# Performance work log

Hardware: AMD Instinct MI355X
Metric: run time of the kernel (lower is better)

Reference implementation:

```python
import jax, jax.numpy as jnp
import numpy as np

N = 50000
E = 1600000
EPS = 1e-16


def transformer_conv(x, src, dst, ea, Wq, bq, Wk, bk, Wv, bv, We, Ws, bs):
    # PyG TransformerConv, heads=1, concat=True, root_weight=True
    C = Wq.shape[1]
    q = x @ Wq + bq                      # [N, C]
    k = x @ Wk + bk                      # [N, C]
    v = x @ Wv + bv                      # [N, C]
    e = ea @ We                          # [E, C]
    k_e = k[src] + e                     # per-edge key
    v_e = v[src] + e                     # per-edge value
    score = (q[dst] * k_e).sum(-1) / jnp.sqrt(jnp.asarray(C, x.dtype))  # [E]
    # segment softmax over incoming edges of each dst node
    m = jax.ops.segment_max(score, dst, num_segments=N)
    ex = jnp.exp(score - m[dst])
    denom = jax.ops.segment_sum(ex, dst, num_segments=N)
    alpha = ex / (denom[dst] + EPS)
    out = jax.ops.segment_sum(alpha[:, None] * v_e, dst, num_segments=N)
    return out + x @ Ws + bs             # skip connection


def gcn_conv(x, src, dst, W, b):
    # PyG GCNConv: self-loops + symmetric deg^-1/2 normalization
    n_idx = jnp.arange(N)
    src2 = jnp.concatenate([src, n_idx])
    dst2 = jnp.concatenate([dst, n_idx])
    deg = jax.ops.segment_sum(jnp.ones(E + N, x.dtype), dst2, num_segments=N)
    dinv = jnp.where(deg > 0, jax.lax.rsqrt(deg), 0.0)
    norm = dinv[src2] * dinv[dst2]       # [E+N]
    h = x @ W                            # [N, out]
    out = jax.ops.segment_sum(norm[:, None] * h[src2], dst2, num_segments=N)
    return out + b


def setup_inputs() -> dict:
    key = jax.random.key(0)
    ks = jax.random.split(key, 32)
    d = {}
    d['x'] = jax.random.normal(ks[0], (N, 128), jnp.float32)
    d['edge_index'] = jax.random.randint(ks[1], (2, E), 0, N, jnp.int64)
    d['edge_attr'] = jax.random.normal(ks[2], (E, 16), jnp.float32)
    shapes = dict(
        Wq1=(128, 96), bq1=(96,), Wk1=(128, 96), bk1=(96,), Wv1=(128, 96), bv1=(96,),
        We1=(16, 96), Ws1=(128, 96), bs1=(96,),
        Wq2=(96, 64), bq2=(64,), Wk2=(96, 64), bk2=(64,), Wv2=(96, 64), bv2=(64,),
        We2=(16, 64), Ws2=(96, 64), bs2=(64,),
        Wmu=(64, 32), bmu=(32,), Wls=(64, 32), bls=(32,))
    for i, (name, shp) in enumerate(shapes.items()):
        scale = 1.0 / np.sqrt(shp[0]) if len(shp) == 2 else 0.02
        d[name] = jax.random.normal(ks[3 + i], shp, jnp.float32) * scale
    return d


def reference(x, edge_index, edge_attr,
              Wq1, bq1, Wk1, bk1, Wv1, bv1, We1, Ws1, bs1,
              Wq2, bq2, Wk2, bk2, Wv2, bv2, We2, Ws2, bs2,
              Wmu, bmu, Wls, bls):
    src, dst = edge_index[0], edge_index[1]
    h = jax.nn.relu(transformer_conv(x, src, dst, edge_attr,
                                     Wq1, bq1, Wk1, bk1, Wv1, bv1, We1, Ws1, bs1))
    h = jax.nn.relu(transformer_conv(h, src, dst, edge_attr,
                                     Wq2, bq2, Wk2, bk2, Wv2, bv2, We2, Ws2, bs2))
    mu = gcn_conv(h, src, dst, Wmu, bmu)
    logstd = gcn_conv(h, src, dst, Wls, bls)
    return mu, logstd
```

## Files before the change

### kernel.cpp

```cpp
#include <hip/hip_runtime.h>
#include <math.h>


#define TPB 256
#define NGRP 8
typedef unsigned int uint32;
typedef unsigned long long u64;
typedef unsigned short u16;
typedef __attribute__((ext_vector_type(4))) float f32x4;
typedef __attribute__((ext_vector_type(4))) uint32 u32x4;
typedef __attribute__((ext_vector_type(4))) int i32x4;
typedef __attribute__((ext_vector_type(8))) short bf16x8;

__device__ __forceinline__ uint32 f2bf(float f) {
    uint32 u = __float_as_uint(f);
    return (u + 0x7fffu + ((u >> 16) & 1u)) >> 16;
}
__device__ __forceinline__ float bf2f(uint32 b) { return __uint_as_float(b << 16); }

__global__ void hist_kernel(const int* __restrict__ dst, int* __restrict__ deg,
                            int E, int span) {
    int grp = blockIdx.x & (NGRP - 1);
    int lo = grp * span;
    int nb = gridDim.x >> 3;
    int bid = blockIdx.x >> 3;
    int stride = nb * TPB * 8;
    for (int base = (bid * TPB + threadIdx.x) * 8; base < E; base += stride) {
        if (base + 8 <= E) {
            i32x4 d0 = __builtin_nontemporal_load((const i32x4*)(dst + base));
            i32x4 d1 = __builtin_nontemporal_load((const i32x4*)(dst + base + 4));
            int dv[8] = {d0.x, d0.y, d0.z, d0.w, d1.x, d1.y, d1.z, d1.w};
#pragma unroll
            for (int u = 0; u < 8; ++u)
                if ((uint32)(dv[u] - lo) < (uint32)span) atomicAdd(&deg[dv[u]], 1);
        } else {
            for (int i = base; i < E; ++i) {
                int d = dst[i];
                if ((uint32)(d - lo) < (uint32)span) atomicAdd(&deg[d], 1);
            }
        }
    }
}

__global__ __launch_bounds__(1024) void scan1_kernel(const int* __restrict__ deg,
                                                     int* __restrict__ prowp,
                                                     int* __restrict__ bsum, int n) {
    __shared__ int wsum[16];
    __shared__ int woff[16];
    int tid = threadIdx.x;
    int i = blockIdx.x * 1024 + tid;
    int lane = tid & 63, w = tid >> 6;
    int dg = (i < n) ? deg[i] : 0;
    int x = (dg + 7) & ~7;
    int v = x;
#pragma unroll
    for (int off = 1; off < 64; off <<= 1) {
        int t = __shfl_up(v, off, 64);
        if (lane >= off) v += t;
    }
    if (lane == 63) wsum[w] = v;
    __syncthreads();
    if (tid < 64) {
        int s = (tid < 16) ? wsum[tid] : 0;
#pragma unroll
        for (int off = 1; off < 16; off <<= 1) {
            int t = __shfl_up(s, off, 64);
            if (lane >= off) s += t;
        }
        if (tid < 16) woff[tid] = s;
    }
    __syncthreads();
    int incl = v + (w ? woff[w - 1] : 0);
    if (i < n) prowp[i] = incl;
    if (tid == 1023) bsum[blockIdx.x] = incl;
}

__global__ void scan2_kernel(const int* __restrict__ bsum, int* __restrict__ boff,
                             int* __restrict__ prowpN, int nb) {
    int tid = threadIdx.x;
    int x = (tid < nb) ? bsum[tid] : 0;
    int v = x;
#pragma unroll
    for (int off = 1; off < 64; off <<= 1) {
        int t = __shfl_up(v, off, 64);
        if (tid >= off) v += t;
    }
    if (tid < nb) boff[tid] = v - x;
    if (tid == nb - 1) *prowpN = v;
}

__global__ __launch_bounds__(1024) void scan3_kernel(const int* __restrict__ deg,
                                                     const int* __restrict__ boff,
                                                     int* __restrict__ prowp,
                                                     int* __restrict__ cursor,
                                                     float* __restrict__ dinv,
                                                     u64* __restrict__ pse, int n) {
    int i = blockIdx.x * 1024 + threadIdx.x;
    if (i < n) {
        int dg = deg[i];
        int x = (dg + 7) & ~7;
        int excl = prowp[i] - x + boff[blockIdx.x];
        prowp[i] = excl;
        cursor[i] = excl;
        dinv[i] = 1.0f / sqrtf((float)(dg + 1));
        u64 pad = (u64)(uint32)n;
        for (int p = excl + dg; p < excl + x; ++p) pse[p] = pad;
    }
}

__global__ void scatter_kernel(const int* __restrict__ src, const int* __restrict__ dst,
                               int* __restrict__ cursor, u64* __restrict__ pse,
                               int E, int span) {
    int grp = blockIdx.x & (NGRP - 1);
    int lo = grp * span;
    int nb = gridDim.x >> 3;
    int bid = blockIdx.x >> 3;
    int stride = nb * TPB * 8;
    for (int base = (bid * TPB + threadIdx.x) * 8; base < E; base += stride) {
        if (base + 8 <= E) {
            i32x4 d0 = __builtin_nontemporal_load((const i32x4*)(dst + base));
            i32x4 d1 = __builtin_nontemporal_load((const i32x4*)(dst + base + 4));
            i32x4 s0 = __builtin_nontemporal_load((const i32x4*)(src + base));
            i32x4 s1 = __builtin_nontemporal_load((const i32x4*)(src + base + 4));
            int dv[8] = {d0.x, d0.y, d0.z, d0.w, d1.x, d1.y, d1.z, d1.w};
            int sv[8] = {s0.x, s0.y, s0.z, s0.w, s1.x, s1.y, s1.z, s1.w};
#pragma unroll
            for (int u = 0; u < 8; ++u) {
                if ((uint32)(dv[u] - lo) < (uint32)span) {
                    int pos = atomicAdd(&cursor[dv[u]], 1);
                    pse[pos] = ((u64)(uint32)(base + u) << 32) | (uint32)sv[u];
                }
            }
        } else {
            for (int i = base; i < E; ++i) {
                int d = dst[i];
                if ((uint32)(d - lo) < (uint32)span) {
                    int pos = atomicAdd(&cursor[d], 1);
                    pse[pos] = ((u64)(uint32)i << 32) | (uint32)src[i];
                }
            }
        }
    }
}

__global__ void permute_kernel(const u64* __restrict__ pse, const float* __restrict__ EA,
                               const int* __restrict__ prowpN,
                               int* __restrict__ psrc, u16* __restrict__ EAb,
                               int N, int cap) {
    int i = blockIdx.x * TPB + threadIdx.x;
    if (i >= cap) return;
    int tot = *prowpN;
    if (i >= tot) return;
    u64 pk = __builtin_nontemporal_load(pse + i);
    uint32 s = (uint32)pk;
    uint32 eid = (uint32)(pk >> 32);
    __builtin_nontemporal_store((int)s, psrc + i);
    u32x4 lo = {0u, 0u, 0u, 0u}, hi = {0u, 0u, 0u, 0u};
    if (s != (uint32)N) {
        const f32x4* e4 = (const f32x4*)(EA + (size_t)eid * 16);
        f32x4 a = __builtin_nontemporal_load(e4);
        f32x4 b = __builtin_nontemporal_load(e4 + 1);
        f32x4 c = __builtin_nontemporal_load(e4 + 2);
        f32x4 d = __builtin_nontemporal_load(e4 + 3);
        lo = (u32x4){f2bf(a.x) | (f2bf(a.y) << 16), f2bf(a.z) | (f2bf(a.w) << 16),
                     f2bf(b.x) | (f2bf(b.y) << 16), f2bf(b.z) | (f2bf(b.w) << 16)};
        hi = (u32x4){f2bf(c.x) | (f2bf(c.y) << 16), f2bf(c.z) | (f2bf(c.w) << 16),
                     f2bf(d.x) | (f2bf(d.y) << 16), f2bf(d.z) | (f2bf(d.w) << 16)};
    }
    u32x4* o = (u32x4*)(EAb + (size_t)i * 16);
    __builtin_nontemporal_store(lo, o);
    __builtin_nontemporal_store(hi, o + 1);
}

__global__ void pack_kernel(
    const float* Wq1, const float* Wk1, const float* Wv1, const float* Ws1,
    const float* bq1, const float* bk1, const float* bv1, const float* bs1,
    const float* We1,
    const float* Wq2, const float* Wk2, const float* Wv2, const float* Ws2,
    const float* bq2, const float* bk2, const float* bv2, const float* bs2,
    const float* We2,
    const float* Wmu, const float* bmu, const float* Wls, const float* bls,
    const float* x, unsigned short* xb, int NX,
    unsigned short* Wc1t, float* bc1, unsigned short* Wc2t, float* bc2,
    float* Wc3, float* bc3) {
    const float s1 = 0.1020620726159658f;
    const float s2 = 0.125f;
    int gi = blockIdx.x * TPB + threadIdx.x;
    const int R0 = 448 * 128, R1 = R0 + 320 * 96, R2 = R1 + 64 * 64;
    const int R3 = R2 + 448, R4 = R3 + 320, R5 = R4 + 64;
    for (int i = gi; i < R5; i += gridDim.x * TPB) {
        if (i < R0) {
            int c = i / 128, kk = i % 128;
            float v = 0.f;
            if (c < 192) {
                int ch = c >> 1;
                v = (c & 1) ? Ws1[kk * 96 + ch] : Wq1[kk * 96 + ch] * s1;
            } else if (c < 208) {
                int t = c - 192; float a = 0.f;
                for (int u = 0; u < 96; ++u) a += Wq1[kk * 96 + u] * We1[t * 96 + u];
                v = a * s1;
            } else if (c < 400) {
                int tt = c - 208;
                v = (tt & 1) ? Wv1[kk * 96 + (tt >> 1)] : Wk1[kk * 96 + (tt >> 1)];
            }
            Wc1t[i] = (unsigned short)f2bf(v);
        } else if (i < R1) {
            int j = i - R0;
            int c = j / 96, kk = j % 96;
            float v = 0.f;
            if (c < 128) {
                int ch = c >> 1;
                v = (c & 1) ? Ws2[kk * 64 + ch] : Wq2[kk * 64 + ch] * s2;
            } else if (c < 144) {
                int t = c - 128; float a = 0.f;
                for (int u = 0; u < 64; ++u) a += Wq2[kk * 64 + u] * We2[t * 64 + u];
                v = a * s2;
            } else if (c < 272) {
                int tt = c - 144;
                v = (tt & 1) ? Wv2[kk * 64 + (tt >> 1)] : Wk2[kk * 64 + (tt >> 1)];
            }
            Wc2t[j] = (unsigned short)f2bf(v);
        } else if (i < R2) {
            int j = i - R1;
            int k = j / 64, c = j % 64;
            Wc3[j] = (c < 32) ? Wmu[k * 32 + c] : Wls[k * 32 + (c - 32)];
        } else if (i < R3) {
            int c = i - R2;
            float v = 0.f;
            if (c < 192) {
                int ch = c >> 1;
                v = (c & 1) ? bs1[ch] : bq1[ch] * s1;
            } else if (c < 208) {
                int t = c - 192; float a = 0.f;
                for (int u = 0; u < 96; ++u) a += bq1[u] * We1[t * 96 + u];
                v = a * s1;
            } else if (c < 400) {
                int tt = c - 208;
                v = (tt & 1) ? bv1[tt >> 1] : bk1[tt >> 1];
            }
            bc1[c] = v;
        } else if (i < R4) {
            int c = i - R3;
            float v = 0.f;
            if (c < 128) {
                int ch = c >> 1;
                v = (c & 1) ? bs2[ch] : bq2[ch] * s2;
            } else if (c < 144) {
                int t = c - 128; float a = 0.f;
                for (int u = 0; u < 64; ++u) a += bq2[u] * We2[t * 64 + u];
                v = a * s2;
            } else if (c < 272) {
                int tt = c - 144;
                v = (tt & 1) ? bv2[tt >> 1] : bk2[tt >> 1];
            }
            bc2[c] = v;
        } else {
            int c = i - R4;
            bc3[c] = (c < 32) ? bmu[c] : bls[c - 32];
        }
    }
    for (int i = gi; i < NX; i += gridDim.x * TPB)
        xb[i] = (unsigned short)f2bf(x[i]);
}

__global__ __launch_bounds__(256) void mfma_gemm_kernel(
    const unsigned short* __restrict__ A,
    const unsigned short* __restrict__ Wt,
    const float* __restrict__ bias,
    uint32* __restrict__ QSp, float* __restrict__ QE,
    uint32* __restrict__ KVp,
    int N, int K, int Cq) {
    __shared__ unsigned short As[64][56];
    __shared__ unsigned short Bs[64][56];
    int r0 = blockIdx.x * 64, c0 = blockIdx.y * 64;
    int tid = threadIdx.x;
    int lane = tid & 63, w = tid >> 6;
    int wm = w >> 1, wn = w & 1;
    int l15 = lane & 15, l4 = lane >> 4;
    f32x4 zero = {0.f, 0.f, 0.f, 0.f};
    f32x4 acc[2][2] = {{zero, zero}, {zero, zero}};
    int sr = tid >> 2, sk = (tid & 3) * 8;

    for (int kc = 0; kc < K; kc += 32) {
        bf16x8 av = {};
        int ar = r0 + sr;
        if (ar < N) av = *(const bf16x8*)(A + (size_t)ar * K + kc + sk);
        *(bf16x8*)&As[sr][sk] = av;
        bf16x8 bv = *(const bf16x8*)(Wt + (size_t)(c0 + sr) * K + kc + sk);
        *(bf16x8*)&Bs[sr][sk] = bv;
        __syncthreads();
        bf16x8 af0 = *(const bf16x8*)&As[32 * wm + l15][l4 * 8];
        bf16x8 af1 = *(const bf16x8*)&As[32 * wm + 16 + l15][l4 * 8];
        bf16x8 bf0 = *(const bf16x8*)&Bs[32 * wn + l15][l4 * 8];
        bf16x8 bf1 = *(const bf16x8*)&Bs[32 * wn + 16 + l15][l4 * 8];
        acc[0][0] = __builtin_amdgcn_mfma_f32_16x16x32_bf16(af0, bf0, acc[0][0], 0, 0, 0);
        acc[0][1] = __builtin_amdgcn_mfma_f32_16x16x32_bf16(af0, bf1, acc[0][1], 0, 0, 0);
        acc[1][0] = __builtin_amdgcn_mfma_f32_16x16x32_bf16(af1, bf0, acc[1][0], 0, 0, 0);
        acc[1][1] = __builtin_amdgcn_mfma_f32_16x16x32_bf16(af1, bf1, acc[1][1], 0, 0, 0);
        __syncthreads();
    }

    int qs0 = 2 * Cq, qe1 = 2 * Cq + 16, kv1 = 4 * Cq + 16;
#pragma unroll
    for (int fm = 0; fm < 2; ++fm) {
#pragma unroll
        for (int fn = 0; fn < 2; ++fn) {
            int cb = c0 + 32 * wn + 16 * fn;
            int c = cb + l15;
            float bia = bias[c];
#pragma unroll
            for (int r = 0; r < 4; ++r) {
                int row = r0 + 32 * wm + 16 * fm + l4 * 4 + r;
                float v = acc[fm][fn][r] + bia;
                float pv = __shfl_xor(v, 1, 64);
                bool ok = (row < N) && !(l15 & 1);
                if (cb < qs0) {
                    if (ok) QSp[(size_t)row * Cq + (c >> 1)] = (f2bf(v) << 16) | f2bf(pv);
                } else if (cb < qe1) {
                    if (row < N) QE[(size_t)row * 16 + (c - qs0)] = v;
                } else if (cb < kv1) {
                    if (ok) {
                        int t = c - qe1;
                        KVp[(size_t)row * Cq + (t >> 1)] = (f2bf(v) << 16) | f2bf(pv);
                    }
                }
            }
        }
    }
}

template <int C>
__global__ __launch_bounds__(256) void edge_attn_kernel(
    const uint32* __restrict__ QSp, const uint32* __restrict__ KVp,
    const u16* __restrict__ EAb, const float* __restrict__ QE,
    const int* __restrict__ prowp, const int* __restrict__ deg,
    const int* __restrict__ psrc, const float* __restrict__ We,
    const float* __restrict__ dinv,
    unsigned short* __restrict__ H1b, uint32* __restrict__ H2p, int N) {
    constexpr int CPL = C / 32;
    int n = blockIdx.x * 4 + (threadIdx.x >> 6);
    if (n >= N) return;
    int lane = threadIdx.x & 63;
    int half = lane >> 5, l = lane & 31, t16 = l & 15;
    bool lo16 = (l < 16);

    uint32 nC = (uint32)n * C;
    float q[CPL], skv[CPL], acc[CPL];
#pragma unroll
    for (int j = 0; j < CPL; ++j) {
        uint32 u = QSp[nC + l + 32 * j];
        q[j] = __uint_as_float(u & 0xffff0000u);
        skv[j] = bf2f(u & 0xffffu);
        acc[j] = 0.f;
    }
    float qe = lo16 ? QE[(uint32)n * 16 + t16] : 0.f;
    float d = 0.f, aea = 0.f;
    int eb = prowp[n], ee = prowp[n + 1];

    for (int base = eb + 8 * half; base < ee; base += 16) {
        const int* sp = psrc + base;
        const u16* ep = EAb + (size_t)base * 16 + t16;
        float dots[8], eav[8];
        uint32 kv[8][CPL];
#pragma unroll
        for (int u = 0; u < 8; ++u) {
            int s = __builtin_nontemporal_load(sp + u);
            eav[u] = bf2f(__builtin_nontemporal_load(ep + u * 16));
            uint32 off = (uint32)s * C + l;
            float dt = qe * eav[u];
#pragma unroll
            for (int j = 0; j < CPL; ++j) {
                uint32 t = KVp[off + 32 * j];
                kv[u][j] = t;
                dt = fmaf(q[j], __uint_as_float(t & 0xffff0000u), dt);
            }
            dots[u] = dt;
        }
#pragma unroll
        for (int a = 0; a < 4; ++a) {
            float x0 = dots[2 * a], x1 = dots[2 * a + 1];
            float z = (lo16 ? x0 : x1) + __shfl_xor(lo16 ? x1 : x0, 16, 64);
            z += __shfl_xor(z, 8, 64);
            z += __shfl_xor(z, 4, 64);
            z += __shfl_xor(z, 2, 64);
            z += __shfl_xor(z, 1, 64);
            float p = __expf(z);
            float p0 = __shfl(p, 0, 32);
            float p1 = __shfl(p, 16, 32);
            d += p0 + p1;
            aea = fmaf(p0, eav[2 * a], fmaf(p1, eav[2 * a + 1], aea));
#pragma unroll
            for (int j = 0; j < CPL; ++j)
                acc[j] = fmaf(p0, __uint_as_float(kv[2 * a][j] << 16),
                         fmaf(p1, __uint_as_float(kv[2 * a + 1][j] << 16), acc[j]));
        }
    }
    d += __shfl_xor(d, 32, 64);
    aea += __shfl_xor(aea, 32, 64);
    d -= (float)((ee - eb) - deg[n]);
    float inv = 1.f / (d + 1e-16f);
    float aeaF = aea * inv;

    float h[CPL];
#pragma unroll
    for (int j = 0; j < CPL; ++j) {
        float s = fmaf(acc[j] + __shfl_xor(acc[j], 32, 64), inv, skv[j]);
        int c = l + 32 * j;
#pragma unroll
        for (int t = 0; t < 16; ++t)
            s = fmaf(__shfl(aeaF, t, 64), We[t * C + c], s);
        h[j] = fmaxf(s, 0.f);
    }
    if (half == 0) {
        if (C == 96) {
#pragma unroll
            for (int j = 0; j < CPL; ++j)
                H1b[nC + l + 32 * j] = (unsigned short)f2bf(h[j]);
        } else {
            float dn = dinv[n];
            H2p[(uint32)n * 32 + l] = f2bf(h[0] * dn) | (f2bf(h[1] * dn) << 16);
        }
    }
}

__global__ __launch_bounds__(256) void gcn_agg_kernel(
    const uint32* __restrict__ H2p, const int* __restrict__ prowp,
    const int* __restrict__ psrc, const float* __restrict__ dinv,
    float* __restrict__ AGG, int N) {
    int n = blockIdx.x * 4 + (threadIdx.x >> 6);
    if (n >= N) return;
    int lane = threadIdx.x & 63, half = lane >> 5, l = lane & 31;
    float s0 = 0.f, s1 = 0.f;
    int eb = prowp[n], ee = prowp[n + 1];
    for (int base = eb + 8 * half; base < ee; base += 16) {
        const int* sp = psrc + base;
#pragma unroll
        for (int u = 0; u < 8; ++u) {
            uint32 s = (uint32)__builtin_nontemporal_load(sp + u);
            uint32 t = H2p[s * 32 + l];
            s0 += bf2f(t & 0xffffu);
            s1 += __uint_as_float(t & 0xffff0000u);
        }
    }
    s0 += __shfl_xor(s0, 32, 64);
    s1 += __shfl_xor(s1, 32, 64);
    if (half == 0) {
        uint32 u = H2p[(uint32)n * 32 + l];
        float dn = dinv[n];
        AGG[(uint32)n * 64 + l]      = dn * (s0 + bf2f(u & 0xffffu));
        AGG[(uint32)n * 64 + 32 + l] = dn * (s1 + __uint_as_float(u & 0xffff0000u));
    }
}

template <int CT, bool SPLIT>
__global__ __launch_bounds__(256) void gemm_kernel(
    const float* __restrict__ A, const float* __restrict__ W,
    const float* __restrict__ bias, float* __restrict__ Out,
    float* __restrict__ Out2, int N, int K, int C) {
    constexpr int TC = CT / 16;
    __shared__ float As[32][68];
    __shared__ float Bs[32][CT + 4];
    int r0 = blockIdx.x * 64, c0 = blockIdx.y * CT;
    int t = threadIdx.x;
    int tr = t >> 4, tc = t & 15;
    float acc[4][TC];
#pragma unroll
    for (int i = 0; i < 4; ++i)
#pragma unroll
        for (int j = 0; j < TC; ++j) acc[i][j] = 0.f;

    for (int kc = 0; kc < K; kc += 32) {
        int ra = t >> 2, kq = (t & 3) * 8;
        float4 a0 = {0, 0, 0, 0}, a1 = {0, 0, 0, 0};
        int r = r0 + ra;
        if (r < N) {
            const float* ap = A + (size_t)r * K + kc + kq;
            a0 = *(const float4*)ap;
            a1 = *(const float4*)(ap + 4);
        }
        As[kq + 0][ra] = a0.x; As[kq + 1][ra] = a0.y;
        As[kq + 2][ra] = a0.z; As[kq + 3][ra] = a0.w;
        As[kq + 4][ra] = a1.x; As[kq + 5][ra] = a1.y;
        As[kq + 6][ra] = a1.z; As[kq + 7][ra] = a1.w;
        constexpr int PASSES = (32 * CT) / (256 * 8);
#pragma unroll
        for (int p = 0; p < PASSES; ++p) {
            int idx = (t + p * 256) * 8;
            int k = idx / CT, c = idx % CT;
            const float* wp = W + (size_t)(kc + k) * C + c0 + c;
            float4 b0 = *(const float4*)wp;
            float4 b1 = *(const float4*)(wp + 4);
            *(float4*)&Bs[k][c] = b0;
            *(float4*)&Bs[k][c + 4] = b1;
        }
        __syncthreads();
#pragma unroll
        for (int k = 0; k < 32; ++k) {
            float4 av = *(const float4*)&As[k][tr * 4];
            float a[4] = {av.x, av.y, av.z, av.w};
#pragma unroll
            for (int u = 0; u < TC / 4; ++u) {
                float4 bv = *(const float4*)&Bs[k][tc * TC + u * 4];
                float b[4] = {bv.x, bv.y, bv.z, bv.w};
#pragma unroll
                for (int i = 0; i < 4; ++i)
#pragma unroll
                    for (int j = 0; j < 4; ++j) acc[i][u * 4 + j] += a[i] * b[j];
            }
        }
        __syncthreads();
    }
#pragma unroll
    for (int i = 0; i < 4; ++i) {
        int r = r0 + tr * 4 + i;
        if (r >= N) continue;
#pragma unroll
        for (int j = 0; j < TC; ++j) {
            int c = c0 + tc * TC + j;
            float v = acc[i][j] + bias[c];
            if (SPLIT) {
                if (c < 32) Out[(size_t)r * 32 + c] = v;
                else        Out2[(size_t)r * 32 + c - 32] = v;
            } else {
                Out[(size_t)r * C + c] = v;
            }
        }
    }
}

extern "C" void kernel_launch(void* const* d_in, const int* in_sizes, int n_in,
                              void* d_out, int out_size, void* d_ws, size_t ws_size,
                              hipStream_t stream) {
    const float* x   = (const float*)d_in[0];
    const int*   ei  = (const int*)d_in[1];
    const float* ea  = (const float*)d_in[2];
    const float* Wq1 = (const float*)d_in[3];  const float* bq1 = (const float*)d_in[4];
    const float* Wk1 = (const float*)d_in[5];  const float* bk1 = (const float*)d_in[6];
    const float* Wv1 = (const float*)d_in[7];  const float* bv1 = (const float*)d_in[8];
    const float* We1 = (const float*)d_in[9];
    const float* Ws1 = (const float*)d_in[10]; const float* bs1 = (const float*)d_in[11];
    const float* Wq2 = (const float*)d_in[12]; const float* bq2 = (const float*)d_in[13];
    const float* Wk2 = (const float*)d_in[14]; const float* bk2 = (const float*)d_in[15];
    const float* Wv2 = (const float*)d_in[16]; const float* bv2 = (const float*)d_in[17];
    const float* We2 = (const float*)d_in[18];
    const float* Ws2 = (const float*)d_in[19]; const float* bs2 = (const float*)d_in[20];
    const float* Wmu = (const float*)d_in[21]; const float* bmu = (const float*)d_in[22];
    const float* Wls = (const float*)d_in[23]; const float* bls = (const float*)d_in[24];

    int N = in_sizes[0] / 128;
    int E = in_sizes[1] / 2;
    const int* src = ei;
    const int* dst = ei + E;
    int E2max = E + 8 * N;
    int span = (N + NGRP - 1) / NGRP;

    char* ws = (char*)d_ws;
    size_t off = 0;
    auto alloc = [&](size_t bytes) -> char* {
        char* p = ws + off;
        off = (off + bytes + 255) & ~(size_t)255;
        return p;
    };
    int*      deg    = (int*)alloc((size_t)N * 4);
    int*      prowp  = (int*)alloc((size_t)(N + 1) * 4);
    int*      cursor = (int*)alloc((size_t)N * 4);
    float*    dinv   = (float*)alloc((size_t)N * 4);
    int*      bsum   = (int*)alloc(256 * 4);
    int*      boff   = (int*)alloc(256 * 4);
    u64*      pse    = (u64*)alloc((size_t)E2max * 8);
    int*      psrc   = (int*)alloc((size_t)E2max * 4);
    u16*      EAb    = (u16*)alloc((size_t)E2max * 16 * 2);
    unsigned short* Wc1t = (unsigned short*)alloc(448 * 128 * 2);
    float*    bc1    = (float*)alloc(448 * 4);
    unsigned short* Wc2t = (unsigned short*)alloc(320 * 96 * 2);
    float*    bc2    = (float*)alloc(320 * 4);
    float*    Wc3    = (float*)alloc(64 * 64 * 4);
    float*    bc3    = (float*)alloc(64 * 4);
    unsigned short* xb = (unsigned short*)alloc((size_t)N * 128 * 2);
    uint32*   QSp  = (uint32*)alloc((size_t)N * 96 * 4);
    float*    QE   = (float*)alloc((size_t)N * 16 * 4);
    uint32*   KVp  = (uint32*)alloc((size_t)(N + 1) * 96 * 4);
    unsigned short* H1b = (unsigned short*)alloc((size_t)N * 96 * 2);
    uint32*   H2p  = (uint32*)alloc((size_t)(N + 1) * 32 * 4);
    float*    AGG  = (float*)alloc((size_t)N * 64 * 4);

    (void)hipMemsetAsync(deg, 0, (size_t)N * 4, stream);
    (void)hipMemsetAsync(KVp + (size_t)N * 96, 0, 96 * 4, stream);
    (void)hipMemsetAsync(H2p + (size_t)N * 32, 0, 32 * 4, stream);

    int e2bk = (E2max + TPB - 1) / TPB;
    int nb1k = (N + 1023) / 1024;
    hist_kernel<<<2048, TPB, 0, stream>>>(dst, deg, E, span);
    scan1_kernel<<<nb1k, 1024, 0, stream>>>(deg, prowp, bsum, N);
    scan2_kernel<<<1, 64, 0, stream>>>(bsum, boff, prowp + N, nb1k);
    scan3_kernel<<<nb1k, 1024, 0, stream>>>(deg, boff, prowp, cursor, dinv, pse, N);
    scatter_kernel<<<2048, TPB, 0, stream>>>(src, dst, cursor, pse, E, span);
    permute_kernel<<<e2bk, TPB, 0, stream>>>(pse, ea, prowp + N, psrc, EAb, N, E2max);
    pack_kernel<<<364, TPB, 0, stream>>>(Wq1, Wk1, Wv1, Ws1, bq1, bk1, bv1, bs1, We1,
                                         Wq2, Wk2, Wv2, Ws2, bq2, bk2, bv2, bs2, We2,
                                         Wmu, bmu, Wls, bls, x, xb, N * 128,
                                         Wc1t, bc1, Wc2t, bc2, Wc3, bc3);

    int rb = (N + 63) / 64;
    int nb4 = (N + 3) / 4;

    mfma_gemm_kernel<<<dim3(rb, 7), 256, 0, stream>>>(xb, Wc1t, bc1, QSp, QE, KVp,
                                                      N, 128, 96);
    edge_attn_kernel<96><<<nb4, 256, 0, stream>>>(QSp, KVp, EAb, QE, prowp, deg, psrc,
                                                  We1, dinv, H1b, nullptr, N);
    mfma_gemm_kernel<<<dim3(rb, 5), 256, 0, stream>>>(H1b, Wc2t, bc2, QSp, QE, KVp,
                                                      N, 96, 64);
    (void)hipMemsetAsync(KVp + (size_t)N * 64, 0, 64 * 4, stream);
    edge_attn_kernel<64><<<nb4, 256, 0, stream>>>(QSp, KVp, EAb, QE, prowp, deg, psrc,
                                                  We2, dinv, nullptr, H2p, N);
    gcn_agg_kernel<<<nb4, 256, 0, stream>>>(H2p, prowp, psrc, dinv, AGG, N);
    gemm_kernel<64, true><<<dim3(rb, 1), 256, 0, stream>>>(AGG, Wc3, bc3, (float*)d_out,
                                                           (float*)d_out + (size_t)N * 32,
                                                           N, 64, 64);
}
```

Baseline: 536.3 us.

## Fuse edge-attribute permutation into CSR scatter and vectorize source index loads

The separate permute kernel and the intermediate packed (edge id, src) array are removed. The scatter kernel now writes the source index and the bf16-converted edge attributes straight to their CSR slot, and scan3 fills the padding slots with the sentinel index and zero attributes. The edge attention and GCN aggregation kernels read eight source indices per iteration with two 16-byte vector loads instead of eight scalar loads. This drops one kernel launch and a full read and write pass over the intermediate array. In exchange the scatter writes are scattered 32-byte stores, and the attribute reads are ordered by edge rather than by CSR position.

```diff
diff --git a/kernel.cpp b/kernel.cpp
--- a/kernel.cpp
+++ b/kernel.cpp
@@ -94,7 +94,8 @@
                                                      int* __restrict__ prowp,
                                                      int* __restrict__ cursor,
                                                      float* __restrict__ dinv,
-                                                     u64* __restrict__ pse, int n) {
+                                                     int* __restrict__ psrc,
+                                                     u16* __restrict__ EAb, int n) {
     int i = blockIdx.x * 1024 + threadIdx.x;
     if (i < n) {
         int dg = deg[i];
@@ -103,13 +104,20 @@
         prowp[i] = excl;
         cursor[i] = excl;
         dinv[i] = 1.0f / sqrtf((float)(dg + 1));
-        u64 pad = (u64)(uint32)n;
-        for (int p = excl + dg; p < excl + x; ++p) pse[p] = pad;
+        u32x4 z = {0u, 0u, 0u, 0u};
+        for (int p = excl + dg; p < excl + x; ++p) {
+            psrc[p] = n;
+            u32x4* o = (u32x4*)(EAb + (size_t)p * 16);
+            o[0] = z;
+            o[1] = z;
+        }
     }
 }
 
 __global__ void scatter_kernel(const int* __restrict__ src, const int* __restrict__ dst,
-                               int* __restrict__ cursor, u64* __restrict__ pse,
+                               const float* __restrict__ EA,
+                               int* __restrict__ cursor,
+                               int* __restrict__ psrc, u16* __restrict__ EAb,
                                int E, int span) {
     int grp = blockIdx.x & (NGRP - 1);
     int lo = grp * span;
@@ -128,7 +136,19 @@
             for (int u = 0; u < 8; ++u) {
                 if ((uint32)(dv[u] - lo) < (uint32)span) {
                     int pos = atomicAdd(&cursor[dv[u]], 1);
-                    pse[pos] = ((u64)(uint32)(base + u) << 32) | (uint32)sv[u];
+                    psrc[pos] = sv[u];
+                    const f32x4* e4 = (const f32x4*)(EA + (size_t)(base + u) * 16);
+                    f32x4 a = __builtin_nontemporal_load(e4);
+                    f32x4 b = __builtin_nontemporal_load(e4 + 1);
+                    f32x4 c = __builtin_nontemporal_load(e4 + 2);
+                    f32x4 d = __builtin_nontemporal_load(e4 + 3);
+                    u32x4 lo4 = {f2bf(a.x) | (f2bf(a.y) << 16), f2bf(a.z) | (f2bf(a.w) << 16),
+                                 f2bf(b.x) | (f2bf(b.y) << 16), f2bf(b.z) | (f2bf(b.w) << 16)};
+                    u32x4 hi4 = {f2bf(c.x) | (f2bf(c.y) << 16), f2bf(c.z) | (f2bf(c.w) << 16),
+                                 f2bf(d.x) | (f2bf(d.y) << 16), f2bf(d.z) | (f2bf(d.w) << 16)};
+                    u32x4* o = (u32x4*)(EAb + (size_t)pos * 16);
+                    o[0] = lo4;
+                    o[1] = hi4;
                 }
             }
         } else {
@@ -136,40 +156,20 @@
                 int d = dst[i];
                 if ((uint32)(d - lo) < (uint32)span) {
                     int pos = atomicAdd(&cursor[d], 1);
-                    pse[pos] = ((u64)(uint32)i << 32) | (uint32)src[i];
+                    psrc[pos] = src[i];
+                    const f32x4* e4 = (const f32x4*)(EA + (size_t)i * 16);
+                    f32x4 a = e4[0], b = e4[1], c = e4[2], dd = e4[3];
+                    u32x4 lo4 = {f2bf(a.x) | (f2bf(a.y) << 16), f2bf(a.z) | (f2bf(a.w) << 16),
+                                 f2bf(b.x) | (f2bf(b.y) << 16), f2bf(b.z) | (f2bf(b.w) << 16)};
+                    u32x4 hi4 = {f2bf(c.x) | (f2bf(c.y) << 16), f2bf(c.z) | (f2bf(c.w) << 16),
+                                 f2bf(dd.x) | (f2bf(dd.y) << 16), f2bf(dd.z) | (f2bf(dd.w) << 16)};
+                    u32x4* o = (u32x4*)(EAb + (size_t)pos * 16);
+                    o[0] = lo4;
+                    o[1] = hi4;
                 }
             }
         }
     }
-}
-
-__global__ void permute_kernel(const u64* __restrict__ pse, const float* __restrict__ EA,
-                               const int* __restrict__ prowpN,
-                               int* __restrict__ psrc, u16* __restrict__ EAb,
-                               int N, int cap) {
-    int i = blockIdx.x * TPB + threadIdx.x;
-    if (i >= cap) return;
-    int tot = *prowpN;
-    if (i >= tot) return;
-    u64 pk = __builtin_nontemporal_load(pse + i);
-    uint32 s = (uint32)pk;
-    uint32 eid = (uint32)(pk >> 32);
-    __builtin_nontemporal_store((int)s, psrc + i);
-    u32x4 lo = {0u, 0u, 0u, 0u}, hi = {0u, 0u, 0u, 0u};
-    if (s != (uint32)N) {
-        const f32x4* e4 = (const f32x4*)(EA + (size_t)eid * 16);
-        f32x4 a = __builtin_nontemporal_load(e4);
-        f32x4 b = __builtin_nontemporal_load(e4 + 1);
-        f32x4 c = __builtin_nontemporal_load(e4 + 2);
-        f32x4 d = __builtin_nontemporal_load(e4 + 3);
-        lo = (u32x4){f2bf(a.x) | (f2bf(a.y) << 16), f2bf(a.z) | (f2bf(a.w) << 16),
-                     f2bf(b.x) | (f2bf(b.y) << 16), f2bf(b.z) | (f2bf(b.w) << 16)};
-        hi = (u32x4){f2bf(c.x) | (f2bf(c.y) << 16), f2bf(c.z) | (f2bf(c.w) << 16),
-                     f2bf(d.x) | (f2bf(d.y) << 16), f2bf(d.z) | (f2bf(d.w) << 16)};
-    }
-    u32x4* o = (u32x4*)(EAb + (size_t)i * 16);
-    __builtin_nontemporal_store(lo, o);
-    __builtin_nontemporal_store(hi, o + 1);
 }
 
 __global__ void pack_kernel(
@@ -358,15 +358,16 @@
     int eb = prowp[n], ee = prowp[n + 1];
 
     for (int base = eb + 8 * half; base < ee; base += 16) {
-        const int* sp = psrc + base;
+        i32x4 s4a = __builtin_nontemporal_load((const i32x4*)(psrc + base));
+        i32x4 s4b = __builtin_nontemporal_load((const i32x4*)(psrc + base + 4));
+        int sv[8] = {s4a.x, s4a.y, s4a.z, s4a.w, s4b.x, s4b.y, s4b.z, s4b.w};
         const u16* ep = EAb + (size_t)base * 16 + t16;
         float dots[8], eav[8];
         uint32 kv[8][CPL];
 #pragma unroll
         for (int u = 0; u < 8; ++u) {
-            int s = __builtin_nontemporal_load(sp + u);
             eav[u] = bf2f(__builtin_nontemporal_load(ep + u * 16));
-            uint32 off = (uint32)s * C + l;
+            uint32 off = (uint32)sv[u] * C + l;
             float dt = qe * eav[u];
 #pragma unroll
             for (int j = 0; j < CPL; ++j) {
@@ -433,11 +434,12 @@
     float s0 = 0.f, s1 = 0.f;
     int eb = prowp[n], ee = prowp[n + 1];
     for (int base = eb + 8 * half; base < ee; base += 16) {
-        const int* sp = psrc + base;
+        i32x4 s4a = __builtin_nontemporal_load((const i32x4*)(psrc + base));
+        i32x4 s4b = __builtin_nontemporal_load((const i32x4*)(psrc + base + 4));
+        int sv[8] = {s4a.x, s4a.y, s4a.z, s4a.w, s4b.x, s4b.y, s4b.z, s4b.w};
 #pragma unroll
         for (int u = 0; u < 8; ++u) {
-            uint32 s = (uint32)__builtin_nontemporal_load(sp + u);
-            uint32 t = H2p[s * 32 + l];
+            uint32 t = H2p[(uint32)sv[u] * 32 + l];
             s0 += bf2f(t & 0xffffu);
             s1 += __uint_as_float(t & 0xffff0000u);
         }
@@ -567,7 +569,6 @@
     float*    dinv   = (float*)alloc((size_t)N * 4);
     int*      bsum   = (int*)alloc(256 * 4);
     int*      boff   = (int*)alloc(256 * 4);
-    u64*      pse    = (u64*)alloc((size_t)E2max * 8);
     int*      psrc   = (int*)alloc((size_t)E2max * 4);
     u16*      EAb    = (u16*)alloc((size_t)E2max * 16 * 2);
     unsigned short* Wc1t = (unsigned short*)alloc(448 * 128 * 2);
@@ -588,14 +589,12 @@
     (void)hipMemsetAsync(KVp + (size_t)N * 96, 0, 96 * 4, stream);
     (void)hipMemsetAsync(H2p + (size_t)N * 32, 0, 32 * 4, stream);
 
-    int e2bk = (E2max + TPB - 1) / TPB;
     int nb1k = (N + 1023) / 1024;
     hist_kernel<<<2048, TPB, 0, stream>>>(dst, deg, E, span);
     scan1_kernel<<<nb1k, 1024, 0, stream>>>(deg, prowp, bsum, N);
     scan2_kernel<<<1, 64, 0, stream>>>(bsum, boff, prowp + N, nb1k);
-    scan3_kernel<<<nb1k, 1024, 0, stream>>>(deg, boff, prowp, cursor, dinv, pse, N);
-    scatter_kernel<<<2048, TPB, 0, stream>>>(src, dst, cursor, pse, E, span);
-    permute_kernel<<<e2bk, TPB, 0, stream>>>(pse, ea, prowp + N, psrc, EAb, N, E2max);
+    scan3_kernel<<<nb1k, 1024, 0, stream>>>(deg, boff, prowp, cursor, dinv, psrc, EAb, N);
+    scatter_kernel<<<2048, TPB, 0, stream>>>(src, dst, ea, cursor, psrc, EAb, E, span);
     pack_kernel<<<364, TPB, 0, stream>>>(Wq1, Wk1, Wv1, Ws1, bq1, bk1, bv1, bs1, We1,
                                          Wq2, Wk2, Wv2, Ws2, bq2, bk2, bv2, bs2, We2,
                                          Wmu, bmu, Wls, bls, x, xb, N * 128,
```

New measurement: 541.9 us. Within noise of the previous version (+1.0%).
